# Kernel optimization log

Hardware: AMD Instinct MI355X
Metric: run time of the kernel (lower is better)

## Reference

```python
import jax, jax.numpy as jnp
import numpy as np
from jax import lax

NTOK, EMB, HID = 33278, 400, 1150
SEQ, BATCH = 70, 80


def _cell(xt, h, c, wi, bi, wh, bh):
    # preact: [B, 4H]; gate order per source: i, f, o, g (g is the LAST slice!)
    p = xt @ wi.T + bi + h @ wh.T + bh
    i = jax.nn.sigmoid(p[:, :HID])
    f = jax.nn.sigmoid(p[:, HID:2 * HID])
    o = jax.nn.sigmoid(p[:, 2 * HID:3 * HID])
    g = jnp.tanh(p[:, 3 * HID:])
    c_t = f * c + i * g
    h_t = o * jnp.tanh(c_t)
    return h_t, c_t


def setup_inputs() -> dict:
    key = jax.random.key(0)
    ks = jax.random.split(key, 16)
    std = 1.0 / np.sqrt(HID)
    u = lambda k, shape: jax.random.uniform(k, shape, jnp.float32, -std, std)
    d = {
        "x": jax.random.randint(ks[0], (SEQ, BATCH), 0, NTOK),
        "h0": jnp.zeros((3, BATCH, HID), jnp.float32),
        "c0": jnp.zeros((3, BATCH, HID), jnp.float32),
        "emb": u(ks[1], (NTOK, EMB)),
        "w_ih1": u(ks[2], (4 * HID, EMB)),  "b_ih1": u(ks[3], (4 * HID,)),
        "w_hh1": u(ks[4], (4 * HID, HID)), "b_hh1": u(ks[5], (4 * HID,)),
        "w_ih2": u(ks[6], (4 * HID, HID)), "b_ih2": u(ks[7], (4 * HID,)),
        "w_hh2": u(ks[8], (4 * HID, HID)), "b_hh2": u(ks[9], (4 * HID,)),
        "w_ih3": u(ks[10], (4 * HID, HID)), "b_ih3": u(ks[11], (4 * HID,)),
        "w_hh3": u(ks[12], (4 * HID, HID)), "b_hh3": u(ks[13], (4 * HID,)),
        "w_dec": u(ks[14], (NTOK, HID)),   "b_dec": u(ks[15], (NTOK,)),
    }
    return d


def reference(x, h0, c0, emb,
              w_ih1, b_ih1, w_hh1, b_hh1,
              w_ih2, b_ih2, w_hh2, b_hh2,
              w_ih3, b_ih3, w_hh3, b_hh3,
              w_dec, b_dec):
    xe = emb[x]  # [S, B, E]

    def step(carry, xt):
        h1, c1, h2, c2, h3, c3 = carry
        h1, c1 = _cell(xt, h1, c1, w_ih1, b_ih1, w_hh1, b_hh1)
        h2, c2 = _cell(h1, h2, c2, w_ih2, b_ih2, w_hh2, b_hh2)
        h3, c3 = _cell(h2, h3, c3, w_ih3, b_ih3, w_hh3, b_hh3)
        return (h1, c1, h2, c2, h3, c3), h3

    carry0 = (h0[0], c0[0], h0[1], c0[1], h0[2], c0[2])
    (h1, c1, h2, c2, h3, c3), zs = lax.scan(step, carry0, xe)  # zs: [S, B, H]

    decoded = zs @ w_dec.T + b_dec  # [S, B, NTOK]
    h = jnp.stack([h1, h2, h3])
    c = jnp.stack([c1, c2, c3])
    return decoded, (h, c)
```

## Files before the change

### kernel.cpp

```cpp
#include <hip/hip_runtime.h>
#include <stdint.h>
#include <math.h>

#define SEQL 70
#define BAT 80
#define EMBD 400
#define HIDD 1150
#define GATES 4600
#define NTOKV 33278
#define MALL 5600
#define KH 1152
#define KE 416
#define N4P 4608
#define NVP 33280
#define NBLK 72
#define KC_H 36
#define HSLAB (80 * KH)
#define KC_E 13
#define XSLAB (80 * KE)
#define WTBLK (4 * 36 * 512)

typedef __bf16 bf16;
typedef bf16 bf16x8 __attribute__((ext_vector_type(8)));
typedef float f32x4 __attribute__((ext_vector_type(4)));

__device__ __forceinline__ float ld_in(const void* p, size_t i, int f32w) {
    return f32w ? ((const float*)p)[i] : (float)((const bf16*)p)[i];
}
__device__ __forceinline__ float clampdiag(float v) {
    return fminf(fmaxf(v, -30000.f), 30000.f);
}
__device__ __forceinline__ void store_h_sc1(bf16* addr, uint32_t bits) {
    asm volatile("global_store_short %0, %1, off sc0 sc1"
                 :: "v"(addr), "v"(bits) : "memory");
}
__device__ __forceinline__ void gload_lds16(const bf16* g, bf16* l) {
    __builtin_amdgcn_global_load_lds(
        (const __attribute__((address_space(1))) void*)g,
        (__attribute__((address_space(3))) void*)l, 16, 0, 0);
}
__device__ __forceinline__ void gload_lds4(const float* g, float* l) {
    __builtin_amdgcn_global_load_lds(
        (const __attribute__((address_space(1))) void*)g,
        (__attribute__((address_space(3))) void*)l, 4, 0, 0);
}
__device__ __forceinline__ size_t tflat(int b, int c, int KC) {
    return (size_t)(b >> 4) * KC * 512 + (size_t)(c >> 5) * 512
         + (size_t)((c >> 3) & 3) * 128 + (size_t)(b & 15) * 8 + (c & 7);
}
__device__ __forceinline__ float fsig(float x) { return 1.f / (1.f + __expf(-x)); }
__device__ __forceinline__ float ftanh(float x) {
    float e = __expf(-2.f * fabsf(x));
    float r = (1.f - e) / (1.f + e);
    return copysignf(r, x);
}

__global__ void detect_dtype(const void* __restrict__ emb, int* __restrict__ flag)
{
    __shared__ int fails;
    if (threadIdx.x == 0) fails = 0;
    __syncthreads();
    const uint32_t* w = (const uint32_t*)emb;
    int f = 0;
    for (int i = threadIdx.x; i < 1024; i += blockDim.x) {
        uint32_t h0 = w[i] & 0xFFFFu;
        uint32_t e0 = (h0 >> 7) & 0xFFu;
        if (e0 > 122u) f++;
    }
    atomicAdd(&fails, f);
    __syncthreads();
    if (threadIdx.x == 0) *flag = (fails > 100) ? 1 : 0;
}

__global__ __launch_bounds__(256)
void gemm_bt(const bf16* __restrict__ A, int KC, int ASLAB,
             const bf16* __restrict__ Bt,
             const float* __restrict__ bias,
             void* __restrict__ Cp, long long ldc,
             int M, int Nout, int outMode, const int* __restrict__ dflag,
             int gx, int gy)
{
    __shared__ __align__(16) bf16 As[3][8 * 512];
    __shared__ __align__(16) bf16 Bs[3][8 * 512];
    const int f32w = *dflag;
    const int tid  = threadIdx.x;
    const int lane = tid & 63;
    const int w    = tid >> 6;

    const int Wb = 32;
    int id = blockIdx.x;
    int fullb = gx / Wb, tw = gx - fullb * Wb;
    int bx, by;
    if (id < fullb * Wb * gy) {
        int band = id / (Wb * gy), wi = id % (Wb * gy);
        bx = band * Wb + wi % Wb;
        by = wi / Wb;
    } else {
        int wi = id - fullb * Wb * gy;
        bx = fullb * Wb + wi % tw;
        by = wi / tw;
    }
    const int bm = by * 128;
    const int bn = bx * 128;

    const int c0 = 2 * w, c1 = 2 * w + 1;
    const int maxrb = M / 16 - 1;
    const int rA0 = min(by * 8 + c0, maxrb);
    const int rA1 = min(by * 8 + c1, maxrb);
    const bf16* gA0 = A + (size_t)(rA0 / 5) * ASLAB + (size_t)(rA0 % 5) * KC * 512 + (size_t)lane * 8;
    const bf16* gA1 = A + (size_t)(rA1 / 5) * ASLAB + (size_t)(rA1 % 5) * KC * 512 + (size_t)lane * 8;
    const bf16* gB0 = Bt + (size_t)(bn / 16 + c0) * KC * 512 + (size_t)lane * 8;
    const bf16* gB1 = Bt + (size_t)(bn / 16 + c1) * KC * 512 + (size_t)lane * 8;

    const int ra = (w >> 1) * 4;
    const int rb = (w & 1) * 4;

    f32x4 acc[4][4] = {};

    auto stage = [&](int kc, int buf) {
        gload_lds16(gA0 + (size_t)kc * 512, &As[buf][c0 * 512]);
        gload_lds16(gA1 + (size_t)kc * 512, &As[buf][c1 * 512]);
        gload_lds16(gB0 + (size_t)kc * 512, &Bs[buf][c0 * 512]);
        gload_lds16(gB1 + (size_t)kc * 512, &Bs[buf][c1 * 512]);
    };
    stage(0, 0);
    if (KC > 1) {
        stage(1, 1);
        asm volatile("s_waitcnt vmcnt(4)" ::: "memory");
    } else {
        asm volatile("s_waitcnt vmcnt(0)" ::: "memory");
    }
    __syncthreads();

    for (int kc = 0; kc < KC; ++kc) {
        const int cur = kc % 3;
        if (kc + 2 < KC) stage(kc + 2, (kc + 2) % 3);
        bf16x8 af[4], bfv[4];
#pragma unroll
        for (int mi = 0; mi < 4; ++mi)
            af[mi] = *(const bf16x8*)&As[cur][(ra + mi) * 512 + lane * 8];
#pragma unroll
        for (int ni = 0; ni < 4; ++ni)
            bfv[ni] = *(const bf16x8*)&Bs[cur][(rb + ni) * 512 + lane * 8];
#pragma unroll
        for (int mi = 0; mi < 4; ++mi)
#pragma unroll
            for (int ni = 0; ni < 4; ++ni)
                acc[mi][ni] = __builtin_amdgcn_mfma_f32_16x16x32_bf16(
                    af[mi], bfv[ni], acc[mi][ni], 0, 0, 0);
        if (kc + 1 < KC) {
            if (kc + 2 < KC)
                asm volatile("s_waitcnt vmcnt(4)" ::: "memory");
            else
                asm volatile("s_waitcnt vmcnt(0)" ::: "memory");
            __syncthreads();
        }
    }

    const int wm = (w >> 1) * 64;
    const int wn = (w & 1) * 64;
    const int lr = lane & 15;
#pragma unroll
    for (int mi = 0; mi < 4; ++mi)
#pragma unroll
        for (int ni = 0; ni < 4; ++ni) {
            int n = bn + wn + ni * 16 + lr;
            if (n >= Nout) continue;
            float bv = bias[n];
#pragma unroll
            for (int rr = 0; rr < 4; ++rr) {
                int mm = bm + wm + mi * 16 + (lane >> 4) * 4 + rr;
                if (mm < M) {
                    float v = clampdiag(acc[mi][ni][rr] + bv);
                    size_t idx = (size_t)mm * ldc + n;
                    if (outMode == 0)      ((float*)Cp)[idx] = v;
                    else if (outMode == 1) ((bf16*)Cp)[idx] = (bf16)v;
                    else {
                        if (f32w) ((float*)Cp)[idx] = v;
                        else      ((bf16*)Cp)[idx] = (bf16)v;
                    }
                }
            }
        }
}

__device__ __forceinline__ void gridbar(int* ctr, int target)
{
    __syncthreads();
    if (threadIdx.x == 0) {
        atomicAdd(ctr, 1);
        int v;
        do {
            asm volatile("global_load_dword %0, %1, off sc0 sc1\n\t"
                         "s_waitcnt vmcnt(0)"
                         : "=v"(v) : "v"(ctr) : "memory");
        } while (v < target);
    }
    __syncthreads();
    asm volatile("" ::: "memory");
}

template<typename GT>
__global__ __launch_bounds__(256, 1)
void lstm_layer(const bf16* __restrict__ WT,
                const GT* __restrict__ G,
                const bf16* __restrict__ H0,
                float* __restrict__ Cst,
                bf16* __restrict__ HA,
                int* __restrict__ ctr)
{
    constexpr bool GF32 = (sizeof(GT) == 4);
    __shared__ __align__(16) float pl4[4][4][5][64][4];
    __shared__ __align__(16) float gl[5][16][64];
    const int tid  = threadIdx.x;
    const int lane = tid & 63;
    const int w    = tid >> 6;
    const int q    = lane >> 4;
    const int lr   = lane & 15;
    const int n0   = blockIdx.x * 16;
    const int jc   = n0 + lr;
    const bool jok = (jc < HIDD);

    const bf16* wtb = WT + (size_t)blockIdx.x * WTBLK + (size_t)(w * 9) * 512
                        + (size_t)lane * 8;
    const int kst = (n0 >> 5) * 512;
    const int qtp = ((n0 & 31) + lr) >> 3;
    const int eo  = lr & 7;

    const int QA = w;
    const bool hasB = (w == 0);
    const int QB = 4;

    float cregA[4], cregB[4];
#pragma unroll
    for (int rr = 0; rr < 4; ++rr) {
        cregA[rr] = jok ? Cst[(size_t)(QA * 16 + q * 4 + rr) * KH + jc] : 0.f;
        cregB[rr] = (hasB && jok) ? Cst[(size_t)(QB * 16 + q * 4 + rr) * KH + jc] : 0.f;
    }

    for (int t = 0; t < SEQL; ++t) {
        const bf16* Hin = t ? (HA + (size_t)(t - 1) * HSLAB) : H0;
        bf16*       HAt = HA + (size_t)t * HSLAB;
        const bf16* hb  = Hin + (size_t)(w * 9) * 512 + (size_t)lane * 8;

        bf16x8 bfr[4][9], a[5][9];
#pragma unroll
        for (int s = 0; s < 4; ++s)
#pragma unroll
            for (int k = 0; k < 9; ++k)
                bfr[s][k] = *(const bf16x8*)(wtb + (size_t)(s * 36 + k) * 512);
#pragma unroll
        for (int mi = 0; mi < 5; ++mi)
#pragma unroll
            for (int k = 0; k < 9; ++k)
                a[mi][k] = *(const bf16x8*)(hb + (size_t)(mi * 36 + k) * 512);

        float gpA[16], gpB[16];
        if constexpr (GF32) {
            const float* gsrc = (const float*)G + (size_t)t * BAT * N4P;
#pragma unroll
            for (int s = 0; s < 4; ++s)
#pragma unroll
                for (int rr = 0; rr < 4; ++rr)
                    gload_lds4(gsrc + (size_t)(QA * 16 + q * 4 + rr) * N4P + s * HIDD + jc,
                               &gl[w][s * 4 + rr][0]);
            if (hasB) {
#pragma unroll
                for (int s = 0; s < 4; ++s)
#pragma unroll
                    for (int rr = 0; rr < 4; ++rr)
                        gload_lds4(gsrc + (size_t)(QB * 16 + q * 4 + rr) * N4P + s * HIDD + jc,
                                   &gl[4][s * 4 + rr][0]);
            }
        } else {
            const GT* gsrc = G + (size_t)t * BAT * N4P;
#pragma unroll
            for (int s = 0; s < 4; ++s)
#pragma unroll
                for (int rr = 0; rr < 4; ++rr) {
                    gpA[s * 4 + rr] = jok ? (float)gsrc[(size_t)(QA * 16 + q * 4 + rr) * N4P + s * HIDD + jc] : 0.f;
                    gpB[s * 4 + rr] = (hasB && jok) ? (float)gsrc[(size_t)(QB * 16 + q * 4 + rr) * N4P + s * HIDD + jc] : 0.f;
                }
        }

        f32x4 acc[4][5] = {};
#pragma unroll
        for (int mi = 0; mi < 5; ++mi)
#pragma unroll
            for (int k = 0; k < 9; ++k)
#pragma unroll
                for (int s = 0; s < 4; ++s)
                    acc[s][mi] = __builtin_amdgcn_mfma_f32_16x16x32_bf16(
                        a[mi][k], bfr[s][k], acc[s][mi], 0, 0, 0);

#pragma unroll
        for (int s = 0; s < 4; ++s)
#pragma unroll
            for (int mi = 0; mi < 5; ++mi)
                *(f32x4*)&pl4[w][s][mi][lane][0] = acc[s][mi];
        __syncthreads();
        if constexpr (GF32)
            asm volatile("s_waitcnt vmcnt(0)" ::: "memory");

        {
            f32x4 p[4];
#pragma unroll
            for (int s = 0; s < 4; ++s)
                p[s] = *(const f32x4*)&pl4[0][s][QA][lane][0]
                     + *(const f32x4*)&pl4[1][s][QA][lane][0]
                     + *(const f32x4*)&pl4[2][s][QA][lane][0]
                     + *(const f32x4*)&pl4[3][s][QA][lane][0];
            if (jok) {
#pragma unroll
                for (int rr = 0; rr < 4; ++rr) {
                    float g0 = GF32 ? gl[w][0 + rr][lane]  : gpA[0 + rr];
                    float g1 = GF32 ? gl[w][4 + rr][lane]  : gpA[4 + rr];
                    float g2 = GF32 ? gl[w][8 + rr][lane]  : gpA[8 + rr];
                    float g3 = GF32 ? gl[w][12 + rr][lane] : gpA[12 + rr];
                    float ii = fsig(p[0][rr] + g0);
                    float ff = fsig(p[1][rr] + g1);
                    float oo = fsig(p[2][rr] + g2);
                    float gg = ftanh(p[3][rr] + g3);
                    float cn = ff * cregA[rr] + ii * gg;
                    cregA[rr] = cn;
                    bf16 hv = (bf16)(oo * ftanh(cn));
                    store_h_sc1(HAt + (size_t)QA * 18432 + kst + qtp * 128 + (q * 4 + rr) * 8 + eo,
                                (uint32_t)__builtin_bit_cast(unsigned short, hv));
                }
            }
        }
        if (hasB) {
            f32x4 p[4];
#pragma unroll
            for (int s = 0; s < 4; ++s)
                p[s] = *(const f32x4*)&pl4[0][s][QB][lane][0]
                     + *(const f32x4*)&pl4[1][s][QB][lane][0]
                     + *(const f32x4*)&pl4[2][s][QB][lane][0]
                     + *(const f32x4*)&pl4[3][s][QB][lane][0];
            if (jok) {
#pragma unroll
                for (int rr = 0; rr < 4; ++rr) {
                    float g0 = GF32 ? gl[4][0 + rr][lane]  : gpB[0 + rr];
                    float g1 = GF32 ? gl[4][4 + rr][lane]  : gpB[4 + rr];
                    float g2 = GF32 ? gl[4][8 + rr][lane]  : gpB[8 + rr];
                    float g3 = GF32 ? gl[4][12 + rr][lane] : gpB[12 + rr];
                    float ii = fsig(p[0][rr] + g0);
                    float ff = fsig(p[1][rr] + g1);
                    float oo = fsig(p[2][rr] + g2);
                    float gg = ftanh(p[3][rr] + g3);
                    float cn = ff * cregB[rr] + ii * gg;
                    cregB[rr] = cn;
                    bf16 hv = (bf16)(oo * ftanh(cn));
                    store_h_sc1(HAt + (size_t)QB * 18432 + kst + qtp * 128 + (q * 4 + rr) * 8 + eo,
                                (uint32_t)__builtin_bit_cast(unsigned short, hv));
                }
            }
        }

        if (t < SEQL - 1) {
            asm volatile("s_waitcnt vmcnt(0)" ::: "memory");
            gridbar(ctr, NBLK * (t + 1));
        }
    }

    if (jok) {
#pragma unroll
        for (int rr = 0; rr < 4; ++rr)
            Cst[(size_t)(QA * 16 + q * 4 + rr) * KH + jc] = cregA[rr];
        if (hasB) {
#pragma unroll
            for (int rr = 0; rr < 4; ++rr)
                Cst[(size_t)(QB * 16 + q * 4 + rr) * KH + jc] = cregB[rr];
        }
    }
}

__global__ void bar_reset(int* ctr) { if (threadIdx.x == 0) *ctr = 0; }

__global__ void pad_wtB(const void* __restrict__ src, bf16* __restrict__ dst,
                        int N, int K, int NB, int KC, const int* __restrict__ dflag)
{
    const int f32w = *dflag;
    size_t total = (size_t)NB * KC * 512;
    for (size_t i = (size_t)blockIdx.x * blockDim.x + threadIdx.x; i < total;
         i += (size_t)gridDim.x * blockDim.x) {
        int o  = (int)(i & 511);
        size_t ci = i >> 9;
        int kc = (int)(ci % KC);
        int nb = (int)(ci / KC);
        int kq = o >> 7, r16 = (o >> 3) & 15, e = o & 7;
        int n = nb * 16 + r16;
        int c = kc * 32 + kq * 8 + e;
        dst[i] = (n < N && c < K) ? (bf16)ld_in(src, (size_t)n * K + c, f32w)
                                  : (bf16)0.f;
    }
}

__global__ void pad_wt(const void* __restrict__ src, bf16* __restrict__ dst,
                       const int* __restrict__ dflag)
{
    const int f32w = *dflag;
    const size_t total = (size_t)NBLK * WTBLK;
    for (size_t i = (size_t)blockIdx.x * blockDim.x + threadIdx.x; i < total;
         i += (size_t)gridDim.x * blockDim.x) {
        int e  = (int)(i & 7);
        int ln = (int)((i >> 3) & 63);
        size_t tile = i >> 9;
        int kg = (int)(tile % 36);
        size_t sb = tile / 36;
        int s   = (int)(sb & 3);
        int blk = (int)(sb >> 2);
        int jr  = blk * 16 + (ln & 15);
        int col = kg * 32 + (ln >> 4) * 8 + e;
        bf16 v = (bf16)0.f;
        if (jr < HIDD && col < HIDD)
            v = (bf16)ld_in(src, (size_t)(s * HIDD + jr) * HIDD + col, f32w);
        dst[i] = v;
    }
}

__global__ void combine_bias(const void* a, const void* b, float* o, int n, int np,
                             const int* __restrict__ dflag)
{
    const int f32w = *dflag;
    int i = blockIdx.x * blockDim.x + threadIdx.x;
    if (i < np) o[i] = (i < n) ? ld_in(a, i, f32w) + ld_in(b, i, f32w) : 0.f;
}

__global__ void cvt_bias(const void* a, float* o, int n, int np,
                         const int* __restrict__ dflag)
{
    const int f32w = *dflag;
    int i = blockIdx.x * blockDim.x + threadIdx.x;
    if (i < np) o[i] = (i < n) ? ld_in(a, i, f32w) : 0.f;
}

__global__ void embed_gather(const int* __restrict__ x, const void* __restrict__ emb,
                             bf16* __restrict__ XE, const int* __restrict__ dflag)
{
    const int f32w = *dflag;
    int row = blockIdx.x;
    int xi  = x[row];
    int b   = row % 80;
    bf16* base = XE + (size_t)(row / 80) * XSLAB;
    for (int c = threadIdx.x; c < KE; c += blockDim.x) {
        float v = (c < EMBD) ? ld_in(emb, (size_t)xi * EMBD + c, f32w) : 0.f;
        base[tflat(b, c, KC_E)] = (bf16)v;
    }
}

__global__ void zero_ha_pad(bf16* HA)
{
    int i = blockIdx.x * blockDim.x + threadIdx.x;
    if (i < MALL * 2) {
        int r = i >> 1;
        int t = r / BAT, b = r - t * BAT;
        int j = HIDD + (i & 1);
        HA[(size_t)t * HSLAB + tflat(b, j, KC_H)] = (bf16)0.f;
    }
}

__global__ void init_state(const void* __restrict__ h0, const void* __restrict__ c0,
                           size_t lofs, bf16* H0buf, float* Cst,
                           const int* __restrict__ dflag)
{
    const int f32w = *dflag;
    int i = blockIdx.x * blockDim.x + threadIdx.x;
    if (i >= BAT * KH) return;
    int b = i / KH, j = i % KH;
    float hv = 0.f, cv = 0.f;
    if (j < HIDD) {
        hv = ld_in(h0, lofs + (size_t)b * HIDD + j, f32w);
        cv = ld_in(c0, lofs + (size_t)b * HIDD + j, f32w);
    }
    H0buf[tflat(b, j, KC_H)] = (bf16)hv;
    Cst[i] = cv;
}

__global__ void write_tail(const bf16* __restrict__ Hfin, const float* __restrict__ Cfin,
                           void* __restrict__ outBase, size_t hOfs, size_t cOfs,
                           const int* __restrict__ dflag)
{
    const int f32w = *dflag;
    int i = blockIdx.x * blockDim.x + threadIdx.x;
    if (i >= BAT * HIDD) return;
    int b = i / HIDD, j = i % HIDD;
    float hv = clampdiag((float)Hfin[tflat(b, j, KC_H)]);
    float cv = clampdiag(Cfin[b * KH + j]);
    if (f32w) {
        ((float*)outBase)[hOfs + i] = hv;
        ((float*)outBase)[cOfs + i] = cv;
    } else {
        ((bf16*)outBase)[hOfs + i] = (bf16)hv;
        ((bf16*)outBase)[cOfs + i] = (bf16)cv;
    }
}

__global__ void sentinel_kernel(void* out, float v, const int* __restrict__ dflag)
{
    if (blockIdx.x == 0 && threadIdx.x == 0) {
        if (*dflag) ((float*)out)[0] = v;
        else        ((bf16*)out)[0] = (bf16)v;
    }
}

extern "C" void kernel_launch(void* const* d_in, const int* in_sizes, int n_in,
                              void* d_out, int out_size, void* d_ws, size_t ws_size,
                              hipStream_t stream)
{
    const int*  x    = (const int*)d_in[0];
    const void* h0   = d_in[1];
    const void* c0   = d_in[2];
    const void* emb  = d_in[3];
    const void* wih[3] = {d_in[4], d_in[8],  d_in[12]};
    const void* bih[3] = {d_in[5], d_in[9],  d_in[13]};
    const void* whh[3] = {d_in[6], d_in[10], d_in[14]};
    const void* bhh[3] = {d_in[7], d_in[11], d_in[15]};
    const void* wdec = d_in[16];
    const void* bdec = d_in[17];
    const size_t DEC = (size_t)MALL * NTOKV;
    (void)in_sizes; (void)n_in; (void)out_size;

    auto al = [](size_t v) { return (v + 255) & ~(size_t)255; };
    const size_t wdecB = al((size_t)NVP * KH * 2);
    auto plan = [&](bool gbf, size_t* offs) -> size_t {
        size_t off = 0;
        auto carve = [&](size_t b) { size_t p = off; off += al(b); return p; };
        offs[0] = carve((size_t)MALL * N4P * (gbf ? 2 : 4));
        offs[1] = carve((size_t)MALL * KE * 2);
        offs[2] = carve((size_t)N4P * KH * 2);
        offs[3] = carve((size_t)NBLK * WTBLK * 2);
        if (off < wdecB) off = wdecB;
        offs[4] = carve((size_t)MALL * KH * 2);
        offs[5] = carve((size_t)N4P * 4);
        offs[6] = carve((size_t)NVP * 4);
        offs[7] = carve((size_t)BAT * KH * 2);
        offs[8] = carve((size_t)BAT * KH * 4);
        offs[9] = carve(256);
        return off;
    };
    size_t offs[10];
    size_t needA = plan(false, offs);
    size_t needB = plan(true, offs);
    bool gbf16;
    if (ws_size >= needA)      { gbf16 = false; plan(false, offs); }
    else if (ws_size >= needB) { gbf16 = true;  plan(true,  offs); }
    else {
        int* dflag = (int*)d_ws;
        detect_dtype<<<1, 256, 0, stream>>>(emb, dflag);
        float mb = (float)(ws_size >> 20);
        if (mb > 20000.f) mb = 20000.f;
        sentinel_kernel<<<1, 64, 0, stream>>>(d_out, 700.f + mb, dflag);
        return;
    }

    char* ws = (char*)d_ws;
    void* G      = ws + offs[0];
    bf16* XE     = (bf16*)(ws + offs[1]);
    bf16* WihP   = (bf16*)(ws + offs[2]);
    bf16* WT     = (bf16*)(ws + offs[3]);
    bf16* WdecP  = (bf16*)(ws + 0);
    bf16* HA     = (bf16*)(ws + offs[4]);
    float* bc    = (float*)(ws + offs[5]);
    float* bd    = (float*)(ws + offs[6]);
    bf16* H0buf  = (bf16*)(ws + offs[7]);
    float* Cst   = (float*)(ws + offs[8]);
    int*  dflag  = (int*)(ws + offs[9]);
    int*  barctr = (int*)(ws + offs[9] + 128);

    detect_dtype<<<1, 256, 0, stream>>>(emb, dflag);
    embed_gather<<<MALL, 128, 0, stream>>>(x, emb, XE, dflag);
    zero_ha_pad<<<(MALL * 2 + 255) / 256, 256, 0, stream>>>(HA);

    for (int l = 0; l < 3; ++l) {
        int Kin = (l == 0) ? EMBD : HIDD;
        int kc  = (l == 0) ? KC_E : KC_H;
        int asl = (l == 0) ? XSLAB : HSLAB;
        pad_wtB<<<2048, 256, 0, stream>>>(wih[l], WihP, GATES, Kin, N4P / 16, kc, dflag);
        pad_wt<<<2048, 256, 0, stream>>>(whh[l], WT, dflag);
        combine_bias<<<(N4P + 255) / 256, 256, 0, stream>>>(bih[l], bhh[l], bc, GATES, N4P, dflag);
        init_state<<<(BAT * KH + 255) / 256, 256, 0, stream>>>(
            h0, c0, (size_t)l * BAT * HIDD, H0buf, Cst, dflag);
        bar_reset<<<1, 64, 0, stream>>>(barctr);
        const bf16* Ain = (l == 0) ? XE : HA;
        {
            int gx = N4P / 128, gy = (MALL + 127) / 128;
            gemm_bt<<<gx * gy, 256, 0, stream>>>(
                Ain, kc, asl, WihP, bc, G, N4P, MALL, N4P,
                gbf16 ? 1 : 0, dflag, gx, gy);
        }
        if (gbf16)
            lstm_layer<bf16><<<NBLK, 256, 0, stream>>>(
                WT, (const bf16*)G, H0buf, Cst, HA, barctr);
        else
            lstm_layer<float><<<NBLK, 256, 0, stream>>>(
                WT, (const float*)G, H0buf, Cst, HA, barctr);
        write_tail<<<(BAT * HIDD + 255) / 256, 256, 0, stream>>>(
            HA + (size_t)(SEQL - 1) * HSLAB, Cst, d_out,
            DEC + (size_t)l * BAT * HIDD,
            DEC + (size_t)3 * BAT * HIDD + (size_t)l * BAT * HIDD, dflag);
    }

    pad_wtB<<<4096, 256, 0, stream>>>(wdec, WdecP, NTOKV, HIDD, NVP / 16, KC_H, dflag);
    cvt_bias<<<(NVP + 255) / 256, 256, 0, stream>>>(bdec, bd, NTOKV, NVP, dflag);
    {
        int gx = NVP / 128, gy = (MALL + 127) / 128;
        gemm_bt<<<gx * gy, 256, 0, stream>>>(
            HA, KC_H, HSLAB, WdecP, bd, d_out, NTOKV, MALL, NTOKV, 2, dflag, gx, gy);
    }
}
```

Baseline: 2.962 ms.

## Enlarge GEMM tiles to 256x256 with 512 threads and double buffering

The shared bf16 GEMM, used for the input-gate projections and the vocabulary decoder, moves from 128x128 tiles with 256 threads and triple-buffered LDS to 256x256 tiles with 512 threads and a single combined double-buffered LDS array. Each wave now computes a 64x128 sub-tile (4x8 MFMA accumulators), which raises arithmetic intensity and cuts global reloads of A and B. Decoder output writes switch to nontemporal stores so the large logits tensor does not pollute cache. The trade-offs are less prefetch depth (one stage ahead with full vmcnt waits), higher register and LDS pressure, and more padded waste on the M edge.

Result: slower. 3.116 ms (+5.2%).

```diff
diff --git a/kernel.cpp b/kernel.cpp
--- a/kernel.cpp
+++ b/kernel.cpp
@@ -72,7 +72,7 @@
     if (threadIdx.x == 0) *flag = (fails > 100) ? 1 : 0;
 }
 
-__global__ __launch_bounds__(256)
+__global__ __launch_bounds__(512, 2)
 void gemm_bt(const bf16* __restrict__ A, int KC, int ASLAB,
              const bf16* __restrict__ Bt,
              const float* __restrict__ bias,
@@ -80,8 +80,7 @@
              int M, int Nout, int outMode, const int* __restrict__ dflag,
              int gx, int gy)
 {
-    __shared__ __align__(16) bf16 As[3][8 * 512];
-    __shared__ __align__(16) bf16 Bs[3][8 * 512];
+    __shared__ __align__(16) bf16 S[2][32 * 512];
     const int f32w = *dflag;
     const int tid  = threadIdx.x;
     const int lane = tid & 63;
@@ -100,84 +99,82 @@
         bx = fullb * Wb + wi % tw;
         by = wi / tw;
     }
-    const int bm = by * 128;
-    const int bn = bx * 128;
-
-    const int c0 = 2 * w, c1 = 2 * w + 1;
+    const int bm = by * 256;
+    const int bn = bx * 256;
+
     const int maxrb = M / 16 - 1;
-    const int rA0 = min(by * 8 + c0, maxrb);
-    const int rA1 = min(by * 8 + c1, maxrb);
-    const bf16* gA0 = A + (size_t)(rA0 / 5) * ASLAB + (size_t)(rA0 % 5) * KC * 512 + (size_t)lane * 8;
-    const bf16* gA1 = A + (size_t)(rA1 / 5) * ASLAB + (size_t)(rA1 % 5) * KC * 512 + (size_t)lane * 8;
-    const bf16* gB0 = Bt + (size_t)(bn / 16 + c0) * KC * 512 + (size_t)lane * 8;
-    const bf16* gB1 = Bt + (size_t)(bn / 16 + c1) * KC * 512 + (size_t)lane * 8;
-
-    const int ra = (w >> 1) * 4;
-    const int rb = (w & 1) * 4;
-
-    f32x4 acc[4][4] = {};
-
+    const bf16* gp[4];
+    const int cbase = w * 4;
+#pragma unroll
+    for (int u = 0; u < 4; ++u) {
+        int c = cbase + u;
+        if (c < 16) {
+            int rb = min(by * 16 + c, maxrb);
+            gp[u] = A + (size_t)(rb / 5) * ASLAB + (size_t)(rb % 5) * KC * 512
+                      + (size_t)lane * 8;
+        } else {
+            gp[u] = Bt + (size_t)(bn / 16 + c - 16) * KC * 512 + (size_t)lane * 8;
+        }
+    }
     auto stage = [&](int kc, int buf) {
-        gload_lds16(gA0 + (size_t)kc * 512, &As[buf][c0 * 512]);
-        gload_lds16(gA1 + (size_t)kc * 512, &As[buf][c1 * 512]);
-        gload_lds16(gB0 + (size_t)kc * 512, &Bs[buf][c0 * 512]);
-        gload_lds16(gB1 + (size_t)kc * 512, &Bs[buf][c1 * 512]);
+#pragma unroll
+        for (int u = 0; u < 4; ++u)
+            gload_lds16(gp[u] + (size_t)kc * 512, &S[buf][(cbase + u) * 512]);
     };
+
+    const int ag = (w & 3) * 4;
+    const int bg = 16 + (w >> 2) * 8;
+
+    f32x4 acc[4][8] = {};
+
     stage(0, 0);
-    if (KC > 1) {
-        stage(1, 1);
-        asm volatile("s_waitcnt vmcnt(4)" ::: "memory");
-    } else {
-        asm volatile("s_waitcnt vmcnt(0)" ::: "memory");
-    }
+    asm volatile("s_waitcnt vmcnt(0)" ::: "memory");
     __syncthreads();
 
     for (int kc = 0; kc < KC; ++kc) {
-        const int cur = kc % 3;
-        if (kc + 2 < KC) stage(kc + 2, (kc + 2) % 3);
-        bf16x8 af[4], bfv[4];
-#pragma unroll
-        for (int mi = 0; mi < 4; ++mi)
-            af[mi] = *(const bf16x8*)&As[cur][(ra + mi) * 512 + lane * 8];
-#pragma unroll
-        for (int ni = 0; ni < 4; ++ni)
-            bfv[ni] = *(const bf16x8*)&Bs[cur][(rb + ni) * 512 + lane * 8];
-#pragma unroll
-        for (int mi = 0; mi < 4; ++mi)
-#pragma unroll
-            for (int ni = 0; ni < 4; ++ni)
-                acc[mi][ni] = __builtin_amdgcn_mfma_f32_16x16x32_bf16(
-                    af[mi], bfv[ni], acc[mi][ni], 0, 0, 0);
+        const int cur = kc & 1;
+        if (kc + 1 < KC) stage(kc + 1, cur ^ 1);
+        bf16x8 af[4], bfv[8];
+#pragma unroll
+        for (int i = 0; i < 4; ++i)
+            af[i] = *(const bf16x8*)&S[cur][(ag + i) * 512 + lane * 8];
+#pragma unroll
+        for (int j = 0; j < 8; ++j)
+            bfv[j] = *(const bf16x8*)&S[cur][(bg + j) * 512 + lane * 8];
+#pragma unroll
+        for (int i = 0; i < 4; ++i)
+#pragma unroll
+            for (int j = 0; j < 8; ++j)
+                acc[i][j] = __builtin_amdgcn_mfma_f32_16x16x32_bf16(
+                    af[i], bfv[j], acc[i][j], 0, 0, 0);
         if (kc + 1 < KC) {
-            if (kc + 2 < KC)
-                asm volatile("s_waitcnt vmcnt(4)" ::: "memory");
-            else
-                asm volatile("s_waitcnt vmcnt(0)" ::: "memory");
+            asm volatile("s_waitcnt vmcnt(0)" ::: "memory");
             __syncthreads();
         }
     }
 
-    const int wm = (w >> 1) * 64;
-    const int wn = (w & 1) * 64;
+    const int q  = lane >> 4;
     const int lr = lane & 15;
-#pragma unroll
-    for (int mi = 0; mi < 4; ++mi)
-#pragma unroll
-        for (int ni = 0; ni < 4; ++ni) {
-            int n = bn + wn + ni * 16 + lr;
+    const int bmw = bm + (w & 3) * 64;
+    const int bnw = bn + (w >> 2) * 128;
+#pragma unroll
+    for (int i = 0; i < 4; ++i)
+#pragma unroll
+        for (int j = 0; j < 8; ++j) {
+            int n = bnw + j * 16 + lr;
             if (n >= Nout) continue;
             float bv = bias[n];
 #pragma unroll
             for (int rr = 0; rr < 4; ++rr) {
-                int mm = bm + wm + mi * 16 + (lane >> 4) * 4 + rr;
+                int mm = bmw + i * 16 + q * 4 + rr;
                 if (mm < M) {
-                    float v = clampdiag(acc[mi][ni][rr] + bv);
+                    float v = clampdiag(acc[i][j][rr] + bv);
                     size_t idx = (size_t)mm * ldc + n;
                     if (outMode == 0)      ((float*)Cp)[idx] = v;
                     else if (outMode == 1) ((bf16*)Cp)[idx] = (bf16)v;
                     else {
-                        if (f32w) ((float*)Cp)[idx] = v;
-                        else      ((bf16*)Cp)[idx] = (bf16)v;
+                        if (f32w) __builtin_nontemporal_store(v, &((float*)Cp)[idx]);
+                        else      __builtin_nontemporal_store((bf16)v, &((bf16*)Cp)[idx]);
                     }
                 }
             }
@@ -584,8 +581,8 @@
         bar_reset<<<1, 64, 0, stream>>>(barctr);
         const bf16* Ain = (l == 0) ? XE : HA;
         {
-            int gx = N4P / 128, gy = (MALL + 127) / 128;
-            gemm_bt<<<gx * gy, 256, 0, stream>>>(
+            int gx = N4P / 256, gy = (MALL + 255) / 256;
+            gemm_bt<<<gx * gy, 512, 0, stream>>>(
                 Ain, kc, asl, WihP, bc, G, N4P, MALL, N4P,
                 gbf16 ? 1 : 0, dflag, gx, gy);
         }
@@ -604,8 +601,8 @@
     pad_wtB<<<4096, 256, 0, stream>>>(wdec, WdecP, NTOKV, HIDD, NVP / 16, KC_H, dflag);
     cvt_bias<<<(NVP + 255) / 256, 256, 0, stream>>>(bdec, bd, NTOKV, NVP, dflag);
     {
-        int gx = NVP / 128, gy = (MALL + 127) / 128;
-        gemm_bt<<<gx * gy, 256, 0, stream>>>(
+        int gx = NVP / 256, gy = (MALL + 255) / 256;
+        gemm_bt<<<gx * gy, 512, 0, stream>>>(
             HA, KC_H, HSLAB, WdecP, bd, d_out, NTOKV, MALL, NTOKV, 2, dflag, gx, gy);
     }
 }
```
